# Optimization experiments

Hardware: AMD Instinct MI355X
Metric: run time of the kernel (lower is better)

The kernel has to match this reference:

```python
import jax, jax.numpy as jnp
import numpy as np

B, Q, K, D = 8, 2048, 2048, 64

def setup_inputs() -> dict:
    key = jax.random.key(0)
    kq, kk, kv, kl = jax.random.split(key, 4)
    queries = jax.random.normal(kq, (B, Q, D), dtype=jnp.float32)
    keys = jax.random.normal(kk, (B, K, D), dtype=jnp.float32)
    values = jax.random.normal(kv, (B, K, D), dtype=jnp.float32)
    valid_lens = jax.random.randint(kl, (B,), 1, K + 1)  # at least 1 valid key
    return {"queries": queries, "keys": keys, "values": values, "valid_lens": valid_lens}

def reference(queries, keys, values, valid_lens):
    d = queries.shape[-1]
    # scores: [B, Q, K]
    scores = jnp.einsum("bqd,bkd->bqk", queries, keys) / jnp.sqrt(jnp.float32(d))
    # d2l-style masked softmax: positions >= valid_len get -1e6 before softmax
    kpos = jnp.arange(scores.shape[-1])  # [K]
    mask = kpos[None, None, :] < valid_lens[:, None, None]  # [B,1,K]
    scores = jnp.where(mask, scores, jnp.float32(-1e6))
    attn = jax.nn.softmax(scores, axis=-1)
    # dropout is identity at inference (training=False)
    return jnp.einsum("bqk,bkd->bqd", attn, values)
```

## Files before the change

kernel.cpp:

```cpp
#include <hip/hip_runtime.h>

typedef float    f32x4  __attribute__((ext_vector_type(4)));
typedef float    f32x16 __attribute__((ext_vector_type(16)));
typedef _Float16 half8  __attribute__((ext_vector_type(8)));

constexpr int NB = 8;
constexpr int NQ = 2048;
constexpr int NKEY = 2048;
constexpr int DD = 64;
constexpr int KB = 32;
constexpr int NT = NKEY / KB;
constexpr size_t TILE_BYTES = 4096;

#define QSCALE (0.125f * 1.44269504088896340736f)

__device__ inline unsigned pkh(float a, float b) {
    return __builtin_bit_cast(unsigned, __builtin_amdgcn_cvt_pkrtz(a, b));
}

__global__ __launch_bounds__(256) void convert_kv(
    const float* __restrict__ Kp, const float* __restrict__ Vp,
    char* __restrict__ Kh, char* __restrict__ Vt)
{
    __shared__ __align__(16) char vbuf[32 * 144];
    const int g    = blockIdx.x;
    const bool isV = (g >= NB * NT);
    const int bt   = isV ? g - NB * NT : g;
    const int tid  = threadIdx.x;
    const int b = bt >> 6, T = bt & 63;

    const int key = tid >> 3;
    const int dc  = (tid & 7) * 8;
    const float* src = (isV ? Vp : Kp)
                     + ((size_t)b * NKEY + T * KB + key) * DD + dc;
    f32x4 f0 = *(const f32x4*)src;
    f32x4 f1 = *(const f32x4*)(src + 4);
    half8 h;
#pragma unroll
    for (int i = 0; i < 4; ++i) {
        h[i]     = (_Float16)f0[i];
        h[4 + i] = (_Float16)f1[i];
    }

    if (!isV) {
        char* dst = Kh + (size_t)bt * TILE_BYTES
                  + (dc >> 4) * 1024 + (((dc >> 3) & 1) * 32 + key) * 16;
        *(half8*)dst = h;
    } else {
        *(half8*)(vbuf + key * 144 + dc * 2) = h;
        __syncthreads();
        const int d  = tid >> 2;
        const int kc = tid & 3;
        half8 o;
#pragma unroll
        for (int j = 0; j < 8; ++j)
            o[j] = *(const _Float16*)(vbuf + (kc * 8 + j) * 144 + d * 2);
        const int frag = (kc >> 1) * 2 + (d >> 5);
        char* dst = Vt + (size_t)bt * TILE_BYTES
                  + frag * 1024 + ((kc & 1) * 32 + (d & 31)) * 16;
        *(half8*)dst = o;
    }
}

__device__ __forceinline__ void pv_frag(
    const f32x16& sv, const half8 (&vf)[4], int hi, f32x16& o0, f32x16& o1)
{
    const unsigned w0 = pkh(sv[0],  sv[1]),  w1 = pkh(sv[2],  sv[3]);
    const unsigned w2 = pkh(sv[4],  sv[5]),  w3 = pkh(sv[6],  sv[7]);
    const unsigned w4 = pkh(sv[8],  sv[9]),  w5 = pkh(sv[10], sv[11]);
    const unsigned w6 = pkh(sv[12], sv[13]), w7 = pkh(sv[14], sv[15]);
    const unsigned p0 = __shfl_xor(w0, 32), p1 = __shfl_xor(w1, 32);
    const unsigned p2 = __shfl_xor(w2, 32), p3 = __shfl_xor(w3, 32);
    const unsigned p4 = __shfl_xor(w4, 32), p5 = __shfl_xor(w5, 32);
    const unsigned p6 = __shfl_xor(w6, 32), p7 = __shfl_xor(w7, 32);
    const bool h1 = (hi != 0);
    union { unsigned u[4]; half8 h; } A0, A1;
    A0.u[0] = h1 ? p2 : w0;  A0.u[1] = h1 ? p3 : w1;
    A0.u[2] = h1 ? w2 : p0;  A0.u[3] = h1 ? w3 : p1;
    A1.u[0] = h1 ? p6 : w4;  A1.u[1] = h1 ? p7 : w5;
    A1.u[2] = h1 ? w6 : p4;  A1.u[3] = h1 ? w7 : p5;

    __builtin_amdgcn_s_setprio(1);
    o0 = __builtin_amdgcn_mfma_f32_32x32x16_f16(A0.h, vf[0], o0, 0, 0, 0);
    o1 = __builtin_amdgcn_mfma_f32_32x32x16_f16(A0.h, vf[1], o1, 0, 0, 0);
    o0 = __builtin_amdgcn_mfma_f32_32x32x16_f16(A1.h, vf[2], o0, 0, 0, 0);
    o1 = __builtin_amdgcn_mfma_f32_32x32x16_f16(A1.h, vf[3], o1, 0, 0, 0);
    __builtin_amdgcn_s_setprio(0);
}

__global__ __launch_bounds__(512, 4) void attn_fused(
    const float* __restrict__ Qp, const char* __restrict__ Kh,
    const char* __restrict__ Vt, const int* __restrict__ VL,
    float* __restrict__ Op)
{
    __shared__ __align__(16) char pool[67584];

    const int tid  = threadIdx.x;
    const int wv   = tid >> 6;
    const int lane = tid & 63;
    const int ql   = lane & 31;
    const int hi   = lane >> 5;

    const int g  = blockIdx.x;
    const int b  = ((g >> 3) & 7) ^ ((g >> 8) << 2);
    const int qt = (g & 7) | (((g >> 6) & 7) << 3);
    const int qbase = qt * 32;

    const int vlen = VL[b];
    const int numt = (vlen + KB - 1) / KB;

    const float* qsrc = Qp + ((size_t)b * NQ + qbase + ql) * DD;
    half8 qf[4];
#pragma unroll
    for (int c = 0; c < 4; ++c) {
        f32x4 f0 = *(const f32x4*)(qsrc + c * 16 + hi * 8);
        f32x4 f1 = *(const f32x4*)(qsrc + c * 16 + hi * 8 + 4);
        half8 h;
#pragma unroll
        for (int j = 0; j < 4; ++j) {
            h[j]     = (_Float16)(f0[j] * QSCALE);
            h[4 + j] = (_Float16)(f1[j] * QSCALE);
        }
        qf[c] = h;
    }

    f32x16 o0 = {}, o1 = {};
    float mrun = -1e30f, lrun = 0.f;

    for (int t = wv; t < numt; t += 8) {
        const int kbase = t * KB;
        const char* kp = Kh + (size_t)(b * NT + t) * TILE_BYTES + lane * 16;
        const char* vp = Vt + (size_t)(b * NT + t) * TILE_BYTES + lane * 16;

        half8 kf[4], vf[4];
#pragma unroll
        for (int c = 0; c < 4; ++c) kf[c] = *(const half8*)(kp + c * 1024);
#pragma unroll
        for (int c = 0; c < 4; ++c) vf[c] = *(const half8*)(vp + c * 1024);

        f32x16 sv = {};
        __builtin_amdgcn_s_setprio(1);
#pragma unroll
        for (int c = 0; c < 4; ++c)
            sv = __builtin_amdgcn_mfma_f32_32x32x16_f16(kf[c], qf[c], sv, 0, 0, 0);
        __builtin_amdgcn_s_setprio(0);

        if (kbase + KB > vlen) {
#pragma unroll
            for (int r = 0; r < 16; ++r) {
                const int krow = (r & 3) + 8 * (r >> 2) + 4 * hi;
                sv[r] = (kbase + krow < vlen) ? sv[r] : -1e30f;
            }
        }

        float mx[16];
#pragma unroll
        for (int r = 0; r < 16; ++r) mx[r] = sv[r];
#pragma unroll
        for (int st = 8; st > 0; st >>= 1)
#pragma unroll
            for (int r = 0; r < st; ++r) mx[r] = fmaxf(mx[r], mx[r + st]);
        float mr = fmaxf(mx[0], __shfl_xor(mx[0], 32));

        if (!__all(mr <= mrun + 8.f)) {
            const float mn = fmaxf(mrun, mr);
            const float alpha = __builtin_amdgcn_exp2f(mrun - mn);
            lrun *= alpha;
            mrun = mn;
#pragma unroll
            for (int r = 0; r < 16; ++r) {
                const int qr = (r & 3) + 8 * (r >> 2) + 4 * hi;
                const float ar = __shfl(alpha, qr);
                o0[r] *= ar;
                o1[r] *= ar;
            }
        }

#pragma unroll
        for (int r = 0; r < 16; ++r)
            sv[r] = __builtin_amdgcn_exp2f(sv[r] - mrun);
        float sx[16];
#pragma unroll
        for (int r = 0; r < 16; ++r) sx[r] = sv[r];
#pragma unroll
        for (int st = 8; st > 0; st >>= 1)
#pragma unroll
            for (int r = 0; r < st; ++r) sx[r] += sx[r + st];
        lrun += sx[0] + __shfl_xor(sx[0], 32);

        pv_frag(sv, vf, hi, o0, o1);
    }

    __syncthreads();
    float* Mb = (float*)(pool + 65536);
    float* Lb = (float*)(pool + 65536 + 1024);
    float (*Obuf)[32][64] = (float (*)[32][64])pool;

    if (hi == 0) { Mb[wv * 32 + ql] = mrun; Lb[wv * 32 + ql] = lrun; }
    __syncthreads();

    float Mtot = -1e30f;
#pragma unroll
    for (int w = 0; w < 8; ++w)
        if (Lb[w * 32 + ql] > 0.f) Mtot = fmaxf(Mtot, Mb[w * 32 + ql]);
    const float wown = (lrun > 0.f) ? __builtin_amdgcn_exp2f(mrun - Mtot) : 0.f;

#pragma unroll
    for (int r = 0; r < 16; ++r) {
        const int qr = (r & 3) + 8 * (r >> 2) + 4 * hi;
        const float wr = __shfl(wown, qr);
        Obuf[wv][qr][ql]      = o0[r] * wr;
        Obuf[wv][qr][ql + 32] = o1[r] * wr;
    }
    __syncthreads();

    {
        const int q  = tid >> 4;
        const int d0 = (tid & 15) * 4;
        float Mq = -1e30f;
#pragma unroll
        for (int w = 0; w < 8; ++w)
            if (Lb[w * 32 + q] > 0.f) Mq = fmaxf(Mq, Mb[w * 32 + q]);
        float Ltot = 0.f;
#pragma unroll
        for (int w = 0; w < 8; ++w) {
            const float lw = Lb[w * 32 + q];
            if (lw > 0.f) Ltot += lw * __builtin_amdgcn_exp2f(Mb[w * 32 + q] - Mq);
        }
        f32x4 acc = {};
#pragma unroll
        for (int w = 0; w < 8; ++w)
            acc += *(const f32x4*)(&Obuf[w][q][d0]);
        const float inv = 1.0f / Ltot;
        f32x4 outv;
#pragma unroll
        for (int j = 0; j < 4; ++j) outv[j] = acc[j] * inv;
        *(f32x4*)(Op + ((size_t)b * NQ + qbase + q) * DD + d0) = outv;
    }
}

extern "C" void kernel_launch(void* const* d_in, const int* in_sizes, int n_in,
                              void* d_out, int out_size, void* d_ws, size_t ws_size,
                              hipStream_t stream) {
    const float* Qp = (const float*)d_in[0];
    const float* Kp = (const float*)d_in[1];
    const float* Vp = (const float*)d_in[2];
    const int*   VL = (const int*)d_in[3];
    float* Op = (float*)d_out;

    char* Kh = (char*)d_ws;
    char* Vt = (char*)d_ws + (size_t)NB * NT * TILE_BYTES;

    hipLaunchKernelGGL(convert_kv, dim3(2 * NB * NT), dim3(256), 0, stream,
                       Kp, Vp, Kh, Vt);
    hipLaunchKernelGGL(attn_fused, dim3(NB * (NQ / 32)), dim3(512), 0, stream,
                       Qp, Kh, Vt, VL, Op);
}
```

Measured before the change: 27.63 us.

## Halve waves per block and process two key tiles per iteration

```diff
diff --git a/kernel.cpp b/kernel.cpp
--- a/kernel.cpp
+++ b/kernel.cpp
@@ -88,12 +88,12 @@
     __builtin_amdgcn_s_setprio(0);
 }
 
-__global__ __launch_bounds__(512, 4) void attn_fused(
+__global__ __launch_bounds__(256, 3) void attn_fused(
     const float* __restrict__ Qp, const char* __restrict__ Kh,
     const char* __restrict__ Vt, const int* __restrict__ VL,
     float* __restrict__ Op)
 {
-    __shared__ __align__(16) char pool[67584];
+    __shared__ __align__(16) char pool[34816];
 
     const int tid  = threadIdx.x;
     const int wv   = tid >> 6;
@@ -127,35 +127,48 @@
     f32x16 o0 = {}, o1 = {};
     float mrun = -1e30f, lrun = 0.f;
 
-    for (int t = wv; t < numt; t += 8) {
+    const char* kbase_p = Kh + (size_t)b * NT * TILE_BYTES + lane * 16;
+    const char* vbase_p = Vt + (size_t)b * NT * TILE_BYTES + lane * 16;
+
+    for (int t = wv * 2; t < numt; t += 8) {
         const int kbase = t * KB;
-        const char* kp = Kh + (size_t)(b * NT + t) * TILE_BYTES + lane * 16;
-        const char* vp = Vt + (size_t)(b * NT + t) * TILE_BYTES + lane * 16;
-
-        half8 kf[4], vf[4];
-#pragma unroll
-        for (int c = 0; c < 4; ++c) kf[c] = *(const half8*)(kp + c * 1024);
-#pragma unroll
-        for (int c = 0; c < 4; ++c) vf[c] = *(const half8*)(vp + c * 1024);
-
-        f32x16 sv = {};
+        const char* kp = kbase_p + (size_t)t * TILE_BYTES;
+        const char* vp = vbase_p + (size_t)t * TILE_BYTES;
+        const size_t boff = (t + 1 < numt) ? TILE_BYTES : 0;
+
+        half8 kfA[4], kfB[4], vfA[4], vfB[4];
+#pragma unroll
+        for (int c = 0; c < 4; ++c) {
+            kfA[c] = *(const half8*)(kp + c * 1024);
+            kfB[c] = *(const half8*)(kp + boff + c * 1024);
+        }
+#pragma unroll
+        for (int c = 0; c < 4; ++c) {
+            vfA[c] = *(const half8*)(vp + c * 1024);
+            vfB[c] = *(const half8*)(vp + boff + c * 1024);
+        }
+
+        f32x16 svA = {}, svB = {};
         __builtin_amdgcn_s_setprio(1);
 #pragma unroll
-        for (int c = 0; c < 4; ++c)
-            sv = __builtin_amdgcn_mfma_f32_32x32x16_f16(kf[c], qf[c], sv, 0, 0, 0);
+        for (int c = 0; c < 4; ++c) {
+            svA = __builtin_amdgcn_mfma_f32_32x32x16_f16(kfA[c], qf[c], svA, 0, 0, 0);
+            svB = __builtin_amdgcn_mfma_f32_32x32x16_f16(kfB[c], qf[c], svB, 0, 0, 0);
+        }
         __builtin_amdgcn_s_setprio(0);
 
-        if (kbase + KB > vlen) {
+        if (kbase + 2 * KB > vlen) {
 #pragma unroll
             for (int r = 0; r < 16; ++r) {
                 const int krow = (r & 3) + 8 * (r >> 2) + 4 * hi;
-                sv[r] = (kbase + krow < vlen) ? sv[r] : -1e30f;
+                svA[r] = (kbase + krow < vlen)      ? svA[r] : -1e30f;
+                svB[r] = (kbase + 32 + krow < vlen) ? svB[r] : -1e30f;
             }
         }
 
         float mx[16];
 #pragma unroll
-        for (int r = 0; r < 16; ++r) mx[r] = sv[r];
+        for (int r = 0; r < 16; ++r) mx[r] = fmaxf(svA[r], svB[r]);
 #pragma unroll
         for (int st = 8; st > 0; st >>= 1)
 #pragma unroll
@@ -177,23 +190,27 @@
         }
 
 #pragma unroll
-        for (int r = 0; r < 16; ++r)
-            sv[r] = __builtin_amdgcn_exp2f(sv[r] - mrun);
+        for (int r = 0; r < 16; ++r) {
+            svA[r] = __builtin_amdgcn_exp2f(svA[r] - mrun);
+            svB[r] = __builtin_amdgcn_exp2f(svB[r] - mrun);
+        }
         float sx[16];
 #pragma unroll
-        for (int r = 0; r < 16; ++r) sx[r] = sv[r];
+        for (int r = 0; r < 16; ++r) sx[r] = svA[r] + svB[r];
 #pragma unroll
         for (int st = 8; st > 0; st >>= 1)
 #pragma unroll
             for (int r = 0; r < st; ++r) sx[r] += sx[r + st];
         lrun += sx[0] + __shfl_xor(sx[0], 32);
 
-        pv_frag(sv, vf, hi, o0, o1);
+        pv_frag(svA, vfA, hi, o0, o1);
+        pv_frag(svB, vfB, hi, o0, o1);
     }
 
     __syncthreads();
-    float* Mb = (float*)(pool + 65536);
-    float* Lb = (float*)(pool + 65536 + 1024);
+    float* Mb = (float*)(pool + 32768);
+    float* Lb = (float*)(pool + 32768 + 512);
+    float* Tb = (float*)(pool + 32768 + 1024);
     float (*Obuf)[32][64] = (float (*)[32][64])pool;
 
     if (hi == 0) { Mb[wv * 32 + ql] = mrun; Lb[wv * 32 + ql] = lrun; }
@@ -201,9 +218,16 @@
 
     float Mtot = -1e30f;
 #pragma unroll
-    for (int w = 0; w < 8; ++w)
+    for (int w = 0; w < 4; ++w)
         if (Lb[w * 32 + ql] > 0.f) Mtot = fmaxf(Mtot, Mb[w * 32 + ql]);
+    float Ltot = 0.f;
+#pragma unroll
+    for (int w = 0; w < 4; ++w) {
+        const float lw = Lb[w * 32 + ql];
+        if (lw > 0.f) Ltot += lw * __builtin_amdgcn_exp2f(Mb[w * 32 + ql] - Mtot);
+    }
     const float wown = (lrun > 0.f) ? __builtin_amdgcn_exp2f(mrun - Mtot) : 0.f;
+    if (wv == 0 && hi == 0) Tb[ql] = Ltot;
 
 #pragma unroll
     for (int r = 0; r < 16; ++r) {
@@ -214,28 +238,12 @@
     }
     __syncthreads();
 
-    {
-        const int q  = tid >> 4;
-        const int d0 = (tid & 15) * 4;
-        float Mq = -1e30f;
-#pragma unroll
-        for (int w = 0; w < 8; ++w)
-            if (Lb[w * 32 + q] > 0.f) Mq = fmaxf(Mq, Mb[w * 32 + q]);
-        float Ltot = 0.f;
-#pragma unroll
-        for (int w = 0; w < 8; ++w) {
-            const float lw = Lb[w * 32 + q];
-            if (lw > 0.f) Ltot += lw * __builtin_amdgcn_exp2f(Mb[w * 32 + q] - Mq);
-        }
-        f32x4 acc = {};
-#pragma unroll
-        for (int w = 0; w < 8; ++w)
-            acc += *(const f32x4*)(&Obuf[w][q][d0]);
-        const float inv = 1.0f / Ltot;
-        f32x4 outv;
-#pragma unroll
-        for (int j = 0; j < 4; ++j) outv[j] = acc[j] * inv;
-        *(f32x4*)(Op + ((size_t)b * NQ + qbase + q) * DD + d0) = outv;
+#pragma unroll
+    for (int k = 0; k < 8; ++k) {
+        const int q = wv * 8 + k;
+        const float sum = Obuf[0][q][lane] + Obuf[1][q][lane]
+                        + Obuf[2][q][lane] + Obuf[3][q][lane];
+        Op[((size_t)b * NQ + qbase + q) * DD + lane] = sum / Tb[q];
     }
 }
 
@@ -253,6 +261,6 @@
 
     hipLaunchKernelGGL(convert_kv, dim3(2 * NB * NT), dim3(256), 0, stream,
                        Kp, Vp, Kh, Vt);
-    hipLaunchKernelGGL(attn_fused, dim3(NB * (NQ / 32)), dim3(512), 0, stream,
+    hipLaunchKernelGGL(attn_fused, dim3(NB * (NQ / 32)), dim3(256), 0, stream,
                        Qp, Kh, Vt, VL, Op);
 }
```

Measured after the change: 25.81 us. -6.6%, faster.
